# Kernel optimization log

Hardware: AMD Instinct MI355X
Metric: run time of the kernel (lower is better)

## Reference

```python
import jax, jax.numpy as jnp
import numpy as np

K_SIZE = 5


def extract_patches(x, k):
    # tf.image.extract_patches with SAME padding, stride 1, rate 1.
    # x: (B, H, W, C) -> (B, H, W, k*k, C), patch index ordered row-major (ki, kj),
    # channels last within each tap, matching TF's depth ordering + reshape.
    B, H, W, C = x.shape
    p = k // 2
    xp = jnp.pad(x, ((0, 0), (p, p), (p, p), (0, 0)))
    views = [xp[:, i:i + H, j:j + W, :] for i in range(k) for j in range(k)]
    return jnp.stack(views, axis=3)


def setup_inputs() -> dict:
    key = jax.random.key(0)
    k1, k2, k3, k4 = jax.random.split(key, 4)
    B, H, W, C = 4, 64, 64, 128
    bin_size = 128
    return {
        "main": jax.random.normal(k1, (B, H, W, C), dtype=jnp.float32),
        "main_value": jax.random.normal(k2, (B, H, W, bin_size), dtype=jnp.float32),
        "ref": jax.random.normal(k3, (B, H, W, C), dtype=jnp.float32),
        "ref_value": jax.random.normal(k4, (B, H, W, bin_size), dtype=jnp.float32),
    }


def reference(main, main_value, ref, ref_value):
    # mode == 'dot'
    k = K_SIZE
    main5 = main[:, :, :, None, :]                 # (B,H,W,1,C)
    main_value5 = main_value[:, :, :, None, :]     # (B,H,W,1,bin)
    ref_stacked = extract_patches(ref, k)          # (B,H,W,k*k,C)
    ref_value_stacked = extract_patches(ref_value, k)  # (B,H,W,k*k,bin)
    # concat the center query itself as an extra key/value slot
    ref_con = jnp.concatenate([ref_stacked, main5], axis=3)        # (B,H,W,k*k+1,C)
    attn = jnp.sum(ref_con * main5, axis=4)                         # (B,H,W,k*k+1)
    attn = jax.nn.softmax(attn, axis=3)
    val_con = jnp.concatenate([ref_value_stacked, main_value5], axis=3)  # (B,H,W,k*k+1,bin)
    out = jnp.sum(attn[..., None] * val_con, axis=3)                # (B,H,W,bin)
    return out
```

## Files before the change

kernel.cpp:

```cpp
#include <hip/hip_runtime.h>
#include <math.h>

typedef _Float16 v8h __attribute__((ext_vector_type(8)));
typedef float    v4f __attribute__((ext_vector_type(4)));

#define VT_OFF  0
#define L_OFF   32768
#define P_OFF   45568
#define SL_OFF  53760
#define LDS_SZ  53888

__device__ __forceinline__ int swz(int r, int c16) {
    return (r << 8) + ((c16 ^ (r & 15)) << 4);
}

__global__ __launch_bounds__(512, 4) void local_attn_direct(
    const float* __restrict__ main_,
    const float* __restrict__ main_value,
    const float* __restrict__ ref,
    const float* __restrict__ ref_value,
    float* __restrict__ out)
{
    __shared__ __align__(16) char S[LDS_SZ];

    const int tid = threadIdx.x;
    const int bid = blockIdx.x;
    const int b  = bid >> 7;
    const int h0 = ((bid >> 3) & 15) << 2;
    const int w0 = (bid & 7) << 3;
    const int lane = tid & 63, w = tid >> 6;
    const int l15 = lane & 15, quad = lane >> 4;
    const int mt = w >> 2, wl = w & 3;

    *(uint4*)(S + P_OFF + tid * 16) = make_uint4(0, 0, 0, 0);

    #pragma unroll
    for (int i = 0; i < 4; ++i) {
        const int tk = (w << 2) + i;
        const int pb = tk & 15;
        const int ch = ((tk >> 4) << 6) + lane;
        float pvv[8];
        #pragma unroll
        for (int j = 0; j < 8; ++j) {
            const int pos = (pb << 3) + j;
            float v = 0.f;
            if (pos < 96) {
                const int hy = pos / 12, hx = pos - hy * 12;
                const int gh = h0 - 2 + hy, gw = w0 - 2 + hx;
                if ((gh >= 0) & (gh < 64) & (gw >= 0) & (gw < 64))
                    v = ref_value[(size_t)((((b << 6) + gh) << 6) + gw) * 128 + ch];
            } else {
                const int t2 = pos - 96;
                v = main_value[(size_t)((((b << 6) + h0 + (t2 >> 3)) << 6) + (w0 + (t2 & 7))) * 128 + ch];
            }
            pvv[j] = v;
        }
        v8h hv;
        #pragma unroll
        for (int j = 0; j < 8; ++j) hv[j] = (_Float16)pvv[j];
        *(v8h*)(S + VT_OFF + swz(ch, pb)) = hv;
    }

    v8h a[4];
    float sq = 0.f;
    {
        const int px = (mt << 4) + l15;
        const float* ap = main_ + (size_t)((((b << 6) + h0 + (px >> 3)) << 6) + (w0 + (px & 7))) * 128;
        #pragma unroll
        for (int ks = 0; ks < 4; ++ks) {
            const float4 v0 = *(const float4*)(ap + (ks << 5) + (quad << 3));
            const float4 v1 = *(const float4*)(ap + (ks << 5) + (quad << 3) + 4);
            const float a8[8] = {v0.x, v0.y, v0.z, v0.w, v1.x, v1.y, v1.z, v1.w};
            #pragma unroll
            for (int j = 0; j < 8; ++j) {
                a[ks][j] = (_Float16)a8[j];
                sq += a8[j] * a8[j];
            }
        }
        if (wl == 0) {
            sq += __shfl_xor(sq, 16);
            sq += __shfl_xor(sq, 32);
            if (quad == 0) *(float*)(S + SL_OFF + (px << 2)) = sq;
        }
    }
    #pragma unroll
    for (int nn = 0; nn < 2; ++nn) {
        const int nt = wl + (nn << 2);
        if (nt < 6) {
            const int hr = (nt << 4) + l15;
            const int hy = hr / 12, hx = hr - hy * 12;
            const int gh = h0 - 2 + hy, gw = w0 - 2 + hx;
            const bool ok = (gh >= 0) & (gh < 64) & (gw >= 0) & (gw < 64);
            const float* bp = ref + (size_t)((((b << 6) + (ok ? gh : 0)) << 6) + (ok ? gw : 0)) * 128;
            v4f acc = {0, 0, 0, 0};
            #pragma unroll
            for (int ks = 0; ks < 4; ++ks) {
                float4 v0 = make_float4(0, 0, 0, 0), v1 = v0;
                if (ok) {
                    v0 = *(const float4*)(bp + (ks << 5) + (quad << 3));
                    v1 = *(const float4*)(bp + (ks << 5) + (quad << 3) + 4);
                }
                const float b8[8] = {v0.x, v0.y, v0.z, v0.w, v1.x, v1.y, v1.z, v1.w};
                v8h bh;
                #pragma unroll
                for (int j = 0; j < 8; ++j) bh[j] = (_Float16)b8[j];
                acc = __builtin_amdgcn_mfma_f32_16x16x32_f16(a[ks], bh, acc, 0, 0, 0);
            }
            #pragma unroll
            for (int j = 0; j < 4; ++j) {
                const int px = (mt << 4) + (quad << 2) + j;
                *(float*)(S + L_OFF + px * 400 + (((nt << 4) + l15) << 2)) = acc[j];
            }
        }
    }
    __syncthreads();

    {
        const int half = lane >> 5, l = lane & 31;
        #pragma unroll
        for (int it = 0; it < 2; ++it) {
            const int t = (w << 2) + (it << 1) + half;
            const int ty = t >> 3, tx = t & 7;
            const bool act = l < 26;
            int col = 0;
            float lg = -INFINITY;
            if (l < 25) {
                const int dy = l / 5 - 2, dx = l % 5 - 2;
                col = (ty + dy + 2) * 12 + (tx + dx + 2);
                lg = *(const float*)(S + L_OFF + t * 400 + (col << 2));
            } else if (l == 25) {
                col = 96 + t;
                lg = *(const float*)(S + SL_OFF + (t << 2));
            }
            float m = lg;
            #pragma unroll
            for (int off = 16; off; off >>= 1) m = fmaxf(m, __shfl_xor(m, off));
            const float e = act ? __expf(lg - m) : 0.f;
            float s = e;
            #pragma unroll
            for (int off = 16; off; off >>= 1) s += __shfl_xor(s, off);
            if (act)
                *(_Float16*)(S + P_OFF + swz(t, col >> 3) + ((col & 7) << 1)) = (_Float16)(e / s);
        }
    }
    __syncthreads();

    {
        const int ntp = wl << 1;
        const int prow = (mt << 4) + l15;
        const int v0r = (ntp << 4) + l15, v1r = v0r + 16;
        v4f acc0 = {0, 0, 0, 0}, acc1 = {0, 0, 0, 0};
        #pragma unroll
        for (int ks = 0; ks < 4; ++ks) {
            const int c16 = (ks << 2) + quad;
            const v8h pa  = *(const v8h*)(S + P_OFF  + swz(prow, c16));
            const v8h vt0 = *(const v8h*)(S + VT_OFF + swz(v0r,  c16));
            const v8h vt1 = *(const v8h*)(S + VT_OFF + swz(v1r,  c16));
            acc0 = __builtin_amdgcn_mfma_f32_16x16x32_f16(pa, vt0, acc0, 0, 0, 0);
            acc1 = __builtin_amdgcn_mfma_f32_16x16x32_f16(pa, vt1, acc1, 0, 0, 0);
        }
        #pragma unroll
        for (int j = 0; j < 4; ++j) {
            const int px = (mt << 4) + (quad << 2) + j;
            const size_t gbase =
                (size_t)((((b << 6) + h0 + (px >> 3)) << 6) + (w0 + (px & 7))) * 128;
            out[gbase + ((ntp    ) << 4) + l15] = acc0[j];
            out[gbase + ((ntp + 1) << 4) + l15] = acc1[j];
        }
    }
}

extern "C" void kernel_launch(void* const* d_in, const int* in_sizes, int n_in,
                              void* d_out, int out_size, void* d_ws, size_t ws_size,
                              hipStream_t stream) {
    const float* main_      = (const float*)d_in[0];
    const float* main_value = (const float*)d_in[1];
    const float* ref        = (const float*)d_in[2];
    const float* ref_value  = (const float*)d_in[3];
    float* out = (float*)d_out;

    dim3 grid(4 * 16 * 8), block(512);
    local_attn_direct<<<grid, block, 0, stream>>>(main_, main_value, ref, ref_value, out);
}
```

Baseline: 98.87 us.

## Load value tiles directly from global memory in PV stage instead of staging in LDS

Removes the up-front LDS staging of the value halo as transposed fp16, and shrinks shared memory from about 53KB to about 21KB. In its place, a small per-position offset table is built, and the PV MFMA stage gathers ref_value/main_value straight from global memory into B fragments. This is meant to allow more resident blocks and to overlap the value loads with the softmax. The cost is that global loads now sit on the MFMA critical path as scalar, strided gathers, and each value element is fetched by several waves rather than once.

```diff
diff --git a/kernel.cpp b/kernel.cpp
--- a/kernel.cpp
+++ b/kernel.cpp
@@ -4,17 +4,17 @@
 typedef _Float16 v8h __attribute__((ext_vector_type(8)));
 typedef float    v4f __attribute__((ext_vector_type(4)));
 
-#define VT_OFF  0
-#define L_OFF   32768
-#define P_OFF   45568
-#define SL_OFF  53760
-#define LDS_SZ  53888
+#define L_OFF   0
+#define P_OFF   12800
+#define SL_OFF  20992
+#define RO_OFF  21120
+#define LDS_SZ  21760
 
 __device__ __forceinline__ int swz(int r, int c16) {
     return (r << 8) + ((c16 ^ (r & 15)) << 4);
 }
 
-__global__ __launch_bounds__(512, 4) void local_attn_direct(
+__global__ __launch_bounds__(512, 4) void local_attn_v3(
     const float* __restrict__ main_,
     const float* __restrict__ main_value,
     const float* __restrict__ ref,
@@ -34,31 +34,19 @@
 
     *(uint4*)(S + P_OFF + tid * 16) = make_uint4(0, 0, 0, 0);
 
-    #pragma unroll
-    for (int i = 0; i < 4; ++i) {
-        const int tk = (w << 2) + i;
-        const int pb = tk & 15;
-        const int ch = ((tk >> 4) << 6) + lane;
-        float pvv[8];
-        #pragma unroll
-        for (int j = 0; j < 8; ++j) {
-            const int pos = (pb << 3) + j;
-            float v = 0.f;
-            if (pos < 96) {
-                const int hy = pos / 12, hx = pos - hy * 12;
-                const int gh = h0 - 2 + hy, gw = w0 - 2 + hx;
-                if ((gh >= 0) & (gh < 64) & (gw >= 0) & (gw < 64))
-                    v = ref_value[(size_t)((((b << 6) + gh) << 6) + gw) * 128 + ch];
-            } else {
-                const int t2 = pos - 96;
-                v = main_value[(size_t)((((b << 6) + h0 + (t2 >> 3)) << 6) + (w0 + (t2 & 7))) * 128 + ch];
-            }
-            pvv[j] = v;
+    if (tid < 128) {
+        const int pos = tid;
+        int off;
+        if (pos < 96) {
+            const int hy = pos / 12, hx = pos - hy * 12;
+            const int gh = h0 - 2 + hy, gw = w0 - 2 + hx;
+            const bool ok = (gh >= 0) & (gh < 64) & (gw >= 0) & (gw < 64);
+            off = ok ? ((((b << 6) + gh) << 6) + gw) * 128 : -1;
+        } else {
+            const int t2 = pos - 96;
+            off = ((((b << 6) + h0 + (t2 >> 3)) << 6) + (w0 + (t2 & 7))) * 128;
         }
-        v8h hv;
-        #pragma unroll
-        for (int j = 0; j < 8; ++j) hv[j] = (_Float16)pvv[j];
-        *(v8h*)(S + VT_OFF + swz(ch, pb)) = hv;
+        *(int*)(S + RO_OFF + (pos << 2)) = off;
     }
 
     v8h a[4];
@@ -146,26 +134,36 @@
     __syncthreads();
 
     {
-        const int ntp = wl << 1;
+        const int ntp  = wl << 1;
+        const int ch0  = (ntp << 4) + l15;
+        const int ch1  = ch0 + 16;
         const int prow = (mt << 4) + l15;
-        const int v0r = (ntp << 4) + l15, v1r = v0r + 16;
         v4f acc0 = {0, 0, 0, 0}, acc1 = {0, 0, 0, 0};
         #pragma unroll
         for (int ks = 0; ks < 4; ++ks) {
-            const int c16 = (ks << 2) + quad;
-            const v8h pa  = *(const v8h*)(S + P_OFF  + swz(prow, c16));
-            const v8h vt0 = *(const v8h*)(S + VT_OFF + swz(v0r,  c16));
-            const v8h vt1 = *(const v8h*)(S + VT_OFF + swz(v1r,  c16));
-            acc0 = __builtin_amdgcn_mfma_f32_16x16x32_f16(pa, vt0, acc0, 0, 0, 0);
-            acc1 = __builtin_amdgcn_mfma_f32_16x16x32_f16(pa, vt1, acc1, 0, 0, 0);
+            const v8h pa = *(const v8h*)(S + P_OFF + swz(prow, (ks << 2) + quad));
+            v8h b0, b1;
+            const int kp = (ks << 5) + (quad << 3);
+            #pragma unroll
+            for (int j = 0; j < 8; ++j) {
+                const int pos = kp + j;
+                const int off = *(const int*)(S + RO_OFF + (pos << 2));
+                const float* bp = (pos < 96) ? ref_value : main_value;
+                const float va = (off >= 0) ? bp[off + ch0] : 0.f;
+                const float vb = (off >= 0) ? bp[off + ch1] : 0.f;
+                b0[j] = (_Float16)va;
+                b1[j] = (_Float16)vb;
+            }
+            acc0 = __builtin_amdgcn_mfma_f32_16x16x32_f16(pa, b0, acc0, 0, 0, 0);
+            acc1 = __builtin_amdgcn_mfma_f32_16x16x32_f16(pa, b1, acc1, 0, 0, 0);
         }
         #pragma unroll
         for (int j = 0; j < 4; ++j) {
             const int px = (mt << 4) + (quad << 2) + j;
             const size_t gbase =
                 (size_t)((((b << 6) + h0 + (px >> 3)) << 6) + (w0 + (px & 7))) * 128;
-            out[gbase + ((ntp    ) << 4) + l15] = acc0[j];
-            out[gbase + ((ntp + 1) << 4) + l15] = acc1[j];
+            out[gbase + ch0] = acc0[j];
+            out[gbase + ch1] = acc1[j];
         }
     }
 }
@@ -180,5 +178,5 @@
     float* out = (float*)d_out;
 
     dim3 grid(4 * 16 * 8), block(512);
-    local_attn_direct<<<grid, block, 0, stream>>>(main_, main_value, ref, ref_value, out);
+    local_attn_v3<<<grid, block, 0, stream>>>(main_, main_value, ref, ref_value, out);
 }
```

After: 101.2 us. +2.3%, slower.
